# Kernel tuning notes

Hardware: AMD Instinct MI355X
Metric: run time of the kernel (lower is better)

The kernel has to match this reference:

```python
import jax, jax.numpy as jnp
import numpy as np
import math

DIM = 1024
NUM_HEADS = 16
SHARED_HEADS = 1
ROUTED_HEADS = 3
HEAD_DIM = DIM // NUM_HEADS
B, N = 2, 2048


def setup_inputs() -> dict:
    key = jax.random.key(0)
    ks = jax.random.split(key, 16)
    s = 1.0 / math.sqrt(DIM)
    inp = {
        "x": jax.random.normal(ks[0], (B, N, DIM), dtype=jnp.float32),
        "Wq": jax.random.uniform(ks[1], (DIM, DIM), minval=-s, maxval=s),
        "bq": jax.random.uniform(ks[2], (DIM,), minval=-s, maxval=s),
        "Wk": jax.random.uniform(ks[3], (DIM, DIM), minval=-s, maxval=s),
        "bk": jax.random.uniform(ks[4], (DIM,), minval=-s, maxval=s),
        "Wv": jax.random.uniform(ks[5], (DIM, DIM), minval=-s, maxval=s),
        "bv": jax.random.uniform(ks[6], (DIM,), minval=-s, maxval=s),
        "Wp": jax.random.uniform(ks[7], (DIM, DIM), minval=-s, maxval=s),
        "bp": jax.random.uniform(ks[8], (DIM,), minval=-s, maxval=s),
        "Wr": jax.random.uniform(ks[9], (NUM_HEADS - SHARED_HEADS, DIM), minval=-s, maxval=s),
        "br": jax.random.uniform(ks[10], (NUM_HEADS - SHARED_HEADS,), minval=-s, maxval=s),
        "Ws": jax.random.uniform(ks[11], (2, DIM), minval=-s, maxval=s),
        "bs": jax.random.uniform(ks[12], (2,), minval=-s, maxval=s),
        # temperature init: log(exp(1/0.24)-1), shape (H,1,1)
        "temperature": jnp.full((NUM_HEADS, 1, 1), float(np.log(np.expm1(1.0 / 0.24))), dtype=jnp.float32),
        "query_embedding": 0.02 * jax.random.normal(ks[13], (NUM_HEADS, 1, HEAD_DIM), dtype=jnp.float32),
    }
    return inp


def reference(x, Wq, bq, Wk, bk, Wv, bv, Wp, bp, Wr, br, Ws, bs, temperature, query_embedding):
    Bsz, Nn, C = x.shape
    H, hd = NUM_HEADS, HEAD_DIM

    def heads(W, b):
        y = x @ W.T + b  # [B,N,C]
        return y.reshape(Bsz, Nn, H, hd).transpose(0, 2, 1, 3)  # [B,H,N,hd]

    q = heads(Wq, bq)
    k = heads(Wk, bk)
    v = heads(Wv, bv)

    q_norm = q / jnp.linalg.norm(q, axis=-1, keepdims=True)
    q_scaled = (q_norm + query_embedding[None]) * jax.nn.softplus(temperature)[None]
    attn = jnp.einsum("bhqd,bhkd->bhqk", q_scaled, k) / math.sqrt(hd)
    attn = jax.nn.softmax(attn, axis=-1)
    h = jnp.einsum("bhqk,bhkd->bhqd", attn, v)
    h = h.transpose(0, 2, 1, 3).reshape(Bsz, Nn, C)  # [B,N,C]

    # routed-head gating
    gates = jax.nn.softmax(h @ Wr.T + br, axis=-1)  # [B,N,H-shared]
    _, idx = jax.lax.top_k(gates, ROUTED_HEADS)
    # NOTE: original uses num_classes=num_heads-shared_heads for one_hot
    mask = jax.nn.one_hot(idx, H - SHARED_HEADS, dtype=gates.dtype).sum(axis=-2)
    routed_gates = gates * mask * ROUTED_HEADS

    sw = jax.nn.softmax(h @ Ws.T + bs, axis=-1)  # [B,N,2]
    shared_gates = sw * SHARED_HEADS
    weight_0 = sw * 2.0
    shared_gates = weight_0[..., 0:1] * shared_gates
    routed_gates = weight_0[..., 1:2] * routed_gates
    masked_gates = jnp.concatenate([shared_gates, routed_gates], axis=-1)

    # einsum('bnc,bnd->bnd') == per-token scalar sum over c times h
    out = h * masked_gates.sum(axis=-1, keepdims=True)
    return out @ Wp.T + bp
```

## Files before the change

kernel.cpp:

```cpp
#include <hip/hip_runtime.h>
#include <hip/hip_bf16.h>

typedef short s16x8 __attribute__((ext_vector_type(8)));
typedef float f32x4 __attribute__((ext_vector_type(4)));
typedef float f32x16 __attribute__((ext_vector_type(16)));

__device__ __forceinline__ float b2f(unsigned short u) {
    union { unsigned int i; float f; } v;
    v.i = ((unsigned int)u) << 16;
    return v.f;
}
__device__ __forceinline__ unsigned int pkbf16(float a, float b) {
    union { __hip_bfloat162 h; unsigned int u; } v;
    v.h = __float22bfloat162_rn(make_float2(a, b));
    return v.u;
}
__device__ __forceinline__ float fast_exp2(float x) {
#if __has_builtin(__builtin_amdgcn_exp2f)
    return __builtin_amdgcn_exp2f(x);
#else
    return exp2f(x);
#endif
}

__device__ __forceinline__ void gl_lds16(const unsigned short* g, unsigned short* l) {
    __builtin_amdgcn_global_load_lds(
        (const __attribute__((address_space(1))) void*)g,
        (__attribute__((address_space(3))) void*)l, 16, 0, 0);
}

__device__ __forceinline__ void perm32swap(unsigned int &a, unsigned int &b) {
    asm("v_permlane32_swap_b32 %0, %1" : "+v"(a), "+v"(b));
}

__device__ __forceinline__ s16x8 mk8(unsigned int a, unsigned int b,
                                     unsigned int c, unsigned int d) {
    union { uint4 u; s16x8 h; } v;
    v.u = make_uint4(a, b, c, d);
    return v.h;
}

__device__ __forceinline__ void cvt8(const float* __restrict__ s,
                                     unsigned short* __restrict__ d, int i) {
    const float* p = s + (size_t)i * 8;
    float4 a = *(const float4*)p;
    float4 b = *(const float4*)(p + 4);
    unsigned int u0 = pkbf16(a.x, a.y), u1 = pkbf16(a.z, a.w);
    unsigned int u2 = pkbf16(b.x, b.y), u3 = pkbf16(b.z, b.w);
    uint4 o = {u0, u1, u2, u3};
    *(uint4*)&d[(size_t)i * 8] = o;
}

__global__ __launch_bounds__(256) void cvt_main(
    const float* __restrict__ x,  const float* __restrict__ Wq,
    const float* __restrict__ Wk, const float* __restrict__ Wv,
    const float* __restrict__ Wr, const float* __restrict__ Ws,
    const float* __restrict__ bq, const float* __restrict__ bk,
    const float* __restrict__ bv,
    unsigned short* __restrict__ xb, unsigned short* __restrict__ wqkv,
    unsigned short* __restrict__ wg, float* __restrict__ bqkv)
{
    int blk = blockIdx.x, t = threadIdx.x;
    if (blk < 2048)      cvt8(x,  xb,             blk * 256 + t);
    else if (blk < 2560) cvt8(Wq, wqkv,           (blk - 2048) * 256 + t);
    else if (blk < 3072) cvt8(Wk, wqkv + 1048576, (blk - 2560) * 256 + t);
    else if (blk < 3584) cvt8(Wv, wqkv + 2097152, (blk - 3072) * 256 + t);
    else if (blk < 3592) { int i = (blk - 3584) * 256 + t; if (i < 1920) cvt8(Wr, wg, i); }
    else if (blk < 3593) { int i = t; cvt8(Ws, wg + 15360, i); }
    else {
        int i = (blk - 3593) * 256 + t;
        bqkv[i] = (i < 1024) ? bq[i] : (i < 2048) ? bk[i - 1024] : bv[i - 2048];
    }
}

__global__ __launch_bounds__(256) void qkv_gemm(
    const unsigned short* __restrict__ A,
    const unsigned short* __restrict__ Bw,
    const float* __restrict__ bias,
    unsigned short* __restrict__ Q, unsigned short* __restrict__ K,
    unsigned short* __restrict__ Vt)
{
    __shared__ __attribute__((aligned(16))) unsigned short As[128 * 64];
    __shared__ __attribute__((aligned(16))) unsigned short Bs[128 * 64];
    const int t = threadIdx.x;
    const int wave = t >> 6, lane = t & 63;
    const int m0 = blockIdx.x * 128, n0 = blockIdx.y * 128;
    const int wm = (wave >> 1) * 64, wn = (wave & 1) * 64;
    const int lr = lane & 15, lq = lane >> 4;
    const int srow = lane >> 3;
    const int scol = (((lane & 7) ^ srow) << 3);

    f32x4 acc[4][4];
#pragma unroll
    for (int i = 0; i < 4; ++i)
#pragma unroll
        for (int j = 0; j < 4; ++j) acc[i][j] = (f32x4){0.f, 0.f, 0.f, 0.f};

    for (int k0 = 0; k0 < 1024; k0 += 64) {
        __syncthreads();
#pragma unroll
        for (int i = 0; i < 4; ++i) {
            int rb = wave * 32 + i * 8;
            gl_lds16(&A[(size_t)(m0 + rb + srow) * 1024 + k0 + scol], &As[rb * 64]);
            gl_lds16(&Bw[(size_t)(n0 + rb + srow) * 1024 + k0 + scol], &Bs[rb * 64]);
        }
        __syncthreads();
#pragma unroll
        for (int kk = 0; kk < 64; kk += 32) {
            const int po = ((((kk >> 3) + lq) ^ (lr & 7)) << 3);
            s16x8 af[4], bf[4];
#pragma unroll
            for (int i = 0; i < 4; ++i)
                af[i] = *(const s16x8*)&As[(wm + i * 16 + lr) * 64 + po];
#pragma unroll
            for (int j = 0; j < 4; ++j)
                bf[j] = *(const s16x8*)&Bs[(wn + j * 16 + lr) * 64 + po];
#pragma unroll
            for (int i = 0; i < 4; ++i)
#pragma unroll
                for (int j = 0; j < 4; ++j)
                    acc[i][j] = __builtin_amdgcn_mfma_f32_16x16x32_bf16(af[i], bf[j], acc[i][j], 0, 0, 0);
        }
    }
    const int kind = n0 >> 10;
    const int nc = n0 & 1023;
    if (kind < 2) {
        unsigned short* Cm = kind ? K : Q;
#pragma unroll
        for (int j = 0; j < 4; ++j) {
            int cl = wn + j * 16 + lr;
            float bv = bias[n0 + cl];
#pragma unroll
            for (int i = 0; i < 4; ++i) {
                int rowb = m0 + wm + i * 16 + lq * 4;
                unsigned int u0 = pkbf16(acc[i][j][0] + bv, acc[i][j][1] + bv);
                unsigned int u1 = pkbf16(acc[i][j][2] + bv, acc[i][j][3] + bv);
                Cm[(size_t)(rowb + 0) * 1024 + nc + cl] = (unsigned short)u0;
                Cm[(size_t)(rowb + 1) * 1024 + nc + cl] = (unsigned short)(u0 >> 16);
                Cm[(size_t)(rowb + 2) * 1024 + nc + cl] = (unsigned short)u1;
                Cm[(size_t)(rowb + 3) * 1024 + nc + cl] = (unsigned short)(u1 >> 16);
            }
        }
    } else {
        const int bb = m0 >> 11;
#pragma unroll
        for (int j = 0; j < 4; ++j) {
            int col = nc + wn + j * 16 + lr;
            int hh = col >> 6, dd = col & 63;
            float bv = bias[n0 + wn + j * 16 + lr];
#pragma unroll
            for (int i = 0; i < 4; ++i) {
                int tokb = m0 + wm + i * 16 + lq * 4;
                int tloc = tokb & 2047;
                uint2 u;
                u.x = pkbf16(acc[i][j][0] + bv, acc[i][j][1] + bv);
                u.y = pkbf16(acc[i][j][2] + bv, acc[i][j][3] + bv);
                *(uint2*)&Vt[((size_t)(bb * 16 + hh) * 64 + dd) * 2048 + tloc] = u;
            }
        }
    }
}

__global__ __launch_bounds__(512, 4) void attn_kernel(
    const unsigned short* __restrict__ Q,
    const unsigned short* __restrict__ Kb,
    const unsigned short* __restrict__ Vt,
    const float* __restrict__ temp,
    const float* __restrict__ qe,
    unsigned short* __restrict__ Hout)
{
    __shared__ __attribute__((aligned(16))) unsigned short Ks[2][2][64 * 64];
    __shared__ __attribute__((aligned(16))) unsigned short Vs[2][2][64 * 64];
    __shared__ float Lred[8][32];
    const int t = threadIdx.x, wave = t >> 6, lane = t & 63;
    const int ws = wave >> 2, wq = wave & 3;
    const int l31 = lane & 31, hi = lane >> 5;
    const int bh = blockIdx.x, b = bh >> 4, h = bh & 15;
    const int q0 = blockIdx.y * 128;
    const int srow = lane >> 3;
    const int scol = (((lane & 7) ^ srow) << 3);
    const int kbase = ws << 10;
    unsigned short* KsF = &Ks[0][0][0];

    auto stageK = [&](int kc, int cb) {
#pragma unroll
        for (int i2 = 0; i2 < 2; ++i2) {
            int rb = wq * 16 + i2 * 8;
            gl_lds16(&Kb[(size_t)(b * 2048 + kbase + kc + rb + srow) * 1024 + h * 64 + scol],
                     &Ks[ws][cb][rb * 64]);
        }
    };
    auto stageV = [&](int kc, int cb) {
#pragma unroll
        for (int i2 = 0; i2 < 2; ++i2) {
            int rb = wq * 16 + i2 * 8;
            gl_lds16(&Vt[((size_t)(b * 16 + h) * 64 + rb + srow) * 2048 + kbase + kc + scol],
                     &Vs[ws][cb][rb * 64]);
        }
    };

    {
        int rb = wave * 16;
        gl_lds16(&Q[(size_t)(b * 2048 + q0 + rb + srow) * 1024 + h * 64 + scol],
                 &KsF[rb * 64]);
        gl_lds16(&Q[(size_t)(b * 2048 + q0 + rb + 8 + srow) * 1024 + h * 64 + scol],
                 &KsF[(rb + 8) * 64]);
    }
    __syncthreads();

    s16x8 qf[4];
#pragma unroll
    for (int kd = 0; kd < 4; ++kd)
        qf[kd] = *(const s16x8*)&KsF[(wq * 32 + l31) * 64 + (((kd * 2 + hi) ^ (l31 & 7)) << 3)];
    __syncthreads();

    stageK(0, 0);
    stageV(0, 0);

    float tv = temp[h];
    float sp = ((tv > 20.f) ? tv : log1pf(__expf(tv))) * 0.18033688f;
    s16x8 aqB[4];
    {
        float v[4][8];
        float ss = 0.f;
#pragma unroll
        for (int kd = 0; kd < 4; ++kd)
#pragma unroll
            for (int e = 0; e < 8; ++e) {
                v[kd][e] = b2f((unsigned short)qf[kd][e]);
                ss += v[kd][e] * v[kd][e];
            }
        ss += __shfl_xor(ss, 32);
        float rn = rsqrtf(ss);
#pragma unroll
        for (int kd = 0; kd < 4; ++kd) {
            const float* qh = qe + h * 64 + kd * 16 + hi * 8;
            unsigned int w0 = pkbf16((v[kd][0] * rn + qh[0]) * sp, (v[kd][1] * rn + qh[1]) * sp);
            unsigned int w1 = pkbf16((v[kd][2] * rn + qh[2]) * sp, (v[kd][3] * rn + qh[3]) * sp);
            unsigned int w2 = pkbf16((v[kd][4] * rn + qh[4]) * sp, (v[kd][5] * rn + qh[5]) * sp);
            unsigned int w3 = pkbf16((v[kd][6] * rn + qh[6]) * sp, (v[kd][7] * rn + qh[7]) * sp);
            aqB[kd] = mk8(w0, w1, w2, w3);
        }
    }

    f32x16 accO[2];
#pragma unroll
    for (int r = 0; r < 16; ++r) { accO[0][r] = 0.f; accO[1][r] = 0.f; }
    float lsum = 0.f;

    for (int it = 0; it < 16; ++it) {
        const int c = it & 1;
        __syncthreads();
        if (it < 15) { stageK((it + 1) * 64, c ^ 1); stageV((it + 1) * 64, c ^ 1); }

#pragma unroll
        for (int jj = 0; jj < 2; ++jj) {
            const int j = jj ^ (wave & 1);

            s16x8 kf[4];
#pragma unroll
            for (int kd = 0; kd < 4; ++kd)
                kf[kd] = *(const s16x8*)&Ks[ws][c][(j * 32 + l31) * 64 + (((kd * 2 + hi) ^ (l31 & 7)) << 3)];
            f32x16 s;
#pragma unroll
            for (int r = 0; r < 16; ++r) s[r] = 0.f;
            __builtin_amdgcn_s_setprio(1);
#pragma unroll
            for (int kd = 0; kd < 4; ++kd)
                s = __builtin_amdgcn_mfma_f32_32x32x16_bf16(kf[kd], aqB[kd], s, 0, 0, 0);
            __builtin_amdgcn_s_setprio(0);

            float p[16];
#pragma unroll
            for (int r = 0; r < 16; ++r) p[r] = fast_exp2(s[r]);
            lsum += (((p[0] + p[1]) + (p[2] + p[3])) + ((p[4] + p[5]) + (p[6] + p[7])))
                  + (((p[8] + p[9]) + (p[10] + p[11])) + ((p[12] + p[13]) + (p[14] + p[15])));
            unsigned int u[8];
#pragma unroll
            for (int g = 0; g < 8; ++g) u[g] = pkbf16(p[2 * g], p[2 * g + 1]);

#pragma unroll
            for (int kh = 0; kh < 2; ++kh) {
                unsigned int a0 = u[4 * kh + 0], b0 = u[4 * kh + 2];
                unsigned int a1 = u[4 * kh + 1], b1 = u[4 * kh + 3];
                perm32swap(a0, b0);
                perm32swap(a1, b1);
                s16x8 pf = mk8(a0, a1, b0, b1);
                const int vb = (((j * 4 + kh * 2 + hi) ^ (l31 & 7)) << 3);
                s16x8 v0 = *(const s16x8*)&Vs[ws][c][(l31) * 64 + vb];
                s16x8 v1 = *(const s16x8*)&Vs[ws][c][(32 + l31) * 64 + vb];
                __builtin_amdgcn_s_setprio(1);
                accO[0] = __builtin_amdgcn_mfma_f32_32x32x16_bf16(pf, v0, accO[0], 0, 0, 0);
                accO[1] = __builtin_amdgcn_mfma_f32_32x32x16_bf16(pf, v1, accO[1], 0, 0, 0);
                __builtin_amdgcn_s_setprio(0);
            }
        }
    }

    lsum += __shfl_xor(lsum, 32);
    if (hi == 0) Lred[wave][l31] = lsum;
    __syncthreads();

    float* mb = (wq < 2) ? (float*)&Ks[0][wq][0] : (float*)&Vs[0][wq - 2][0];
    if (ws == 1) {
#pragma unroll
        for (int jd = 0; jd < 2; ++jd)
#pragma unroll
            for (int rg = 0; rg < 4; ++rg) {
                f32x4 vv = { accO[jd][rg * 4 + 0], accO[jd][rg * 4 + 1],
                             accO[jd][rg * 4 + 2], accO[jd][rg * 4 + 3] };
                *(f32x4*)&mb[((jd * 4 + rg) << 8) + (lane << 2)] = vv;
            }
    }
    __syncthreads();
    if (ws == 0) {
#pragma unroll
        for (int jd = 0; jd < 2; ++jd)
#pragma unroll
            for (int rg = 0; rg < 4; ++rg) {
                f32x4 vv = *(const f32x4*)&mb[((jd * 4 + rg) << 8) + (lane << 2)];
                accO[jd][rg * 4 + 0] += vv[0];
                accO[jd][rg * 4 + 1] += vv[1];
                accO[jd][rg * 4 + 2] += vv[2];
                accO[jd][rg * 4 + 3] += vv[3];
            }
#pragma unroll
        for (int jd = 0; jd < 2; ++jd)
#pragma unroll
            for (int r = 0; r < 16; ++r) {
                int qrow = (r & 3) + 8 * (r >> 2) + 4 * hi;
                float inv = 1.f / (Lred[wq][qrow] + Lred[wq + 4][qrow]);
                float val = accO[jd][r] * inv;
                Hout[(size_t)(b * 2048 + q0 + wq * 32 + qrow) * 1024 + h * 64 + jd * 32 + l31] =
                    (unsigned short)pkbf16(val, val);
            }
    }
}

__global__ __launch_bounds__(256) void gate_g(
    const unsigned short* __restrict__ Hb,
    const unsigned short* __restrict__ Wg,
    const float* __restrict__ br, const float* __restrict__ bs,
    const float* __restrict__ Wp, unsigned short* __restrict__ wpb,
    float* __restrict__ g)
{
    __shared__ __attribute__((aligned(16))) unsigned short As[4][16 * 64];
    __shared__ __attribute__((aligned(16))) unsigned short Gs[4][32 * 64];
    __shared__ float Lred[4][16][32];
    const int t = threadIdx.x, wave = t >> 6, lane = t & 63;
    const int lr = lane & 15, lq = lane >> 4;
    const int m0 = blockIdx.x * 16;
    const int srow = lane >> 3;
    const int scol = (((lane & 7) ^ srow) << 3);

    cvt8(Wp, wpb, blockIdx.x * 512 + t);
    cvt8(Wp, wpb, blockIdx.x * 512 + 256 + t);

    f32x4 acc[2];
    acc[0] = (f32x4){0.f, 0.f, 0.f, 0.f};
    acc[1] = (f32x4){0.f, 0.f, 0.f, 0.f};

    for (int k0 = wave * 64; k0 < 1024; k0 += 256) {
        gl_lds16(&Hb[(size_t)(m0 + srow) * 1024 + k0 + scol], &As[wave][0]);
        gl_lds16(&Hb[(size_t)(m0 + 8 + srow) * 1024 + k0 + scol], &As[wave][8 * 64]);
#pragma unroll
        for (int i = 0; i < 4; ++i) {
            int row = i * 8 + srow;
            int wr = (row > 16) ? 16 : row;
            gl_lds16(&Wg[(size_t)wr * 1024 + k0 + scol], &Gs[wave][i * 8 * 64]);
        }
        asm volatile("s_waitcnt vmcnt(0)" ::: "memory");
#pragma unroll
        for (int kk = 0; kk < 64; kk += 32) {
            const int po = ((((kk >> 3) + lq) ^ (lr & 7)) << 3);
            s16x8 af = *(const s16x8*)&As[wave][lr * 64 + po];
#pragma unroll
            for (int j = 0; j < 2; ++j) {
                s16x8 gf = *(const s16x8*)&Gs[wave][(j * 16 + lr) * 64 + po];
                acc[j] = __builtin_amdgcn_mfma_f32_16x16x32_bf16(af, gf, acc[j], 0, 0, 0);
            }
        }
    }
#pragma unroll
    for (int j = 0; j < 2; ++j)
#pragma unroll
        for (int r = 0; r < 4; ++r)
            Lred[wave][lq * 4 + r][j * 16 + lr] = acc[j][r];
    __syncthreads();
    if (t < 16) {
        float lg[17];
#pragma unroll
        for (int j = 0; j < 17; ++j)
            lg[j] = Lred[0][t][j] + Lred[1][t][j] + Lred[2][t][j] + Lred[3][t][j]
                  + ((j < 15) ? br[j] : bs[j - 15]);
        float mx = lg[0];
#pragma unroll
        for (int j = 1; j < 15; ++j) mx = fmaxf(mx, lg[j]);
        float sum = 0.f, v1 = -1.f, v2 = -1.f, v3 = -1.f;
#pragma unroll
        for (int j = 0; j < 15; ++j) {
            float e = __expf(lg[j] - mx);
            sum += e;
            if (e > v1)      { v3 = v2; v2 = v1; v1 = e; }
            else if (e > v2) { v3 = v2; v2 = e; }
            else if (e > v3) { v3 = e; }
        }
        float tops = (v1 + v2 + v3) / sum;
        float sm = fmaxf(lg[15], lg[16]);
        float e0 = __expf(lg[15] - sm), e1 = __expf(lg[16] - sm);
        float inv = 1.f / (e0 + e1);
        g[m0 + t] = 2.f * (e0 * inv) + 6.f * (e1 * inv) * tops;
    }
}

__global__ __launch_bounds__(256) void gemm64_out(
    const unsigned short* __restrict__ A,
    const unsigned short* __restrict__ Bw,
    const float* __restrict__ bias,
    const float* __restrict__ g,
    float* __restrict__ C)
{
    __shared__ __attribute__((aligned(16))) unsigned short As[2][64 * 64];
    __shared__ __attribute__((aligned(16))) unsigned short Bs[2][64 * 64];
    const int t = threadIdx.x, wave = t >> 6, lane = t & 63;
    const int lr = lane & 15, lq = lane >> 4;
    const int m0 = blockIdx.x * 64, n0 = blockIdx.y * 64;
    const int wm = (wave >> 1) * 32, wn = (wave & 1) * 32;
    const int srow = lane >> 3;
    const int scol = (((lane & 7) ^ srow) << 3);

    auto stage = [&](int k0, int cb) {
#pragma unroll
        for (int i = 0; i < 2; ++i) {
            int rb = wave * 16 + i * 8;
            gl_lds16(&A[(size_t)(m0 + rb + srow) * 1024 + k0 + scol], &As[cb][rb * 64]);
            gl_lds16(&Bw[(size_t)(n0 + rb + srow) * 1024 + k0 + scol], &Bs[cb][rb * 64]);
        }
    };

    f32x4 acc[2][2];
#pragma unroll
    for (int i = 0; i < 2; ++i)
#pragma unroll
        for (int j = 0; j < 2; ++j) acc[i][j] = (f32x4){0.f, 0.f, 0.f, 0.f};

    stage(0, 0);
    for (int it = 0; it < 16; ++it) {
        const int c = it & 1;
        __syncthreads();
        if (it < 15) stage((it + 1) * 64, c ^ 1);
#pragma unroll
        for (int kk = 0; kk < 64; kk += 32) {
            const int po = ((((kk >> 3) + lq) ^ (lr & 7)) << 3);
            s16x8 af[2], bf[2];
#pragma unroll
            for (int i = 0; i < 2; ++i)
                af[i] = *(const s16x8*)&As[c][(wm + i * 16 + lr) * 64 + po];
#pragma unroll
            for (int j = 0; j < 2; ++j)
                bf[j] = *(const s16x8*)&Bs[c][(wn + j * 16 + lr) * 64 + po];
#pragma unroll
            for (int i = 0; i < 2; ++i)
#pragma unroll
                for (int j = 0; j < 2; ++j)
                    acc[i][j] = __builtin_amdgcn_mfma_f32_16x16x32_bf16(af[i], bf[j], acc[i][j], 0, 0, 0);
        }
    }
#pragma unroll
    for (int i = 0; i < 2; ++i) {
        const float4 gi = *(const float4*)&g[m0 + wm + i * 16 + lq * 4];
        float gv[4] = {gi.x, gi.y, gi.z, gi.w};
#pragma unroll
        for (int j = 0; j < 2; ++j) {
            int col = n0 + wn + j * 16 + lr;
            float bv = bias[col];
            int rowb = m0 + wm + i * 16 + lq * 4;
#pragma unroll
            for (int r = 0; r < 4; ++r)
                C[(size_t)(rowb + r) * 1024 + col] = acc[i][j][r] * gv[r] + bv;
        }
    }
}

extern "C" void kernel_launch(void* const* d_in, const int* in_sizes, int n_in,
                              void* d_out, int out_size, void* d_ws, size_t ws_size,
                              hipStream_t stream)
{
    (void)in_sizes; (void)n_in; (void)out_size; (void)ws_size;
    const float* x   = (const float*)d_in[0];
    const float* Wq  = (const float*)d_in[1];
    const float* bq  = (const float*)d_in[2];
    const float* Wk  = (const float*)d_in[3];
    const float* bk  = (const float*)d_in[4];
    const float* Wv  = (const float*)d_in[5];
    const float* bv  = (const float*)d_in[6];
    const float* Wp  = (const float*)d_in[7];
    const float* bp  = (const float*)d_in[8];
    const float* Wr  = (const float*)d_in[9];
    const float* br  = (const float*)d_in[10];
    const float* Ws  = (const float*)d_in[11];
    const float* bs  = (const float*)d_in[12];
    const float* temperature = (const float*)d_in[13];
    const float* qe  = (const float*)d_in[14];
    float* out = (float*)d_out;

    const size_t MB = 1048576;
    unsigned short* qb   = (unsigned short*)d_ws;
    unsigned short* kb   = (unsigned short*)((char*)d_ws + 8 * MB);
    unsigned short* hb   = (unsigned short*)((char*)d_ws + 16 * MB);
    unsigned short* wqkv = (unsigned short*)((char*)d_ws + 24 * MB);
    unsigned short* wg   = (unsigned short*)((char*)d_ws + 30 * MB);
    float*          bqkv = (float*)((char*)d_ws + 30 * MB + 65536);
    float*          gbuf = (float*)((char*)d_ws + 30 * MB + 131072);
    unsigned short* xb = (unsigned short*)d_out;
    unsigned short* vt = xb + 4 * MB;
    unsigned short* wpb = qb;

    dim3 blk(256);
    cvt_main<<<dim3(3605), blk, 0, stream>>>(x, Wq, Wk, Wv, Wr, Ws, bq, bk, bv,
                                             xb, wqkv, wg, bqkv);
    qkv_gemm<<<dim3(32, 24), blk, 0, stream>>>(xb, wqkv, bqkv, qb, kb, vt);
    attn_kernel<<<dim3(32, 16), dim3(512), 0, stream>>>(qb, kb, vt, temperature, qe, hb);
    gate_g<<<dim3(256), blk, 0, stream>>>(hb, wg, br, bs, Wp, wpb, gbuf);
    gemm64_out<<<dim3(64, 16), blk, 0, stream>>>(hb, wpb, bp, gbuf, out);
}
```

Before: 213.0 us.

## Double-buffer QKV GEMM with BK=32 and remap block IDs for XCD locality

```diff
diff --git a/kernel.cpp b/kernel.cpp
--- a/kernel.cpp
+++ b/kernel.cpp
@@ -80,15 +80,26 @@
     unsigned short* __restrict__ Q, unsigned short* __restrict__ K,
     unsigned short* __restrict__ Vt)
 {
-    __shared__ __attribute__((aligned(16))) unsigned short As[128 * 64];
-    __shared__ __attribute__((aligned(16))) unsigned short Bs[128 * 64];
+    __shared__ __attribute__((aligned(16))) unsigned short As[2][128 * 32];
+    __shared__ __attribute__((aligned(16))) unsigned short Bs[2][128 * 32];
     const int t = threadIdx.x;
     const int wave = t >> 6, lane = t & 63;
-    const int m0 = blockIdx.x * 128, n0 = blockIdx.y * 128;
+    int bid = blockIdx.y * 32 + blockIdx.x;
+    bid = (bid & 7) * 96 + (bid >> 3);
+    const int m0 = (bid & 31) * 128, n0 = (bid >> 5) * 128;
     const int wm = (wave >> 1) * 64, wn = (wave & 1) * 64;
     const int lr = lane & 15, lq = lane >> 4;
-    const int srow = lane >> 3;
-    const int scol = (((lane & 7) ^ srow) << 3);
+    const int srow = lane >> 2;
+    const int scol = (((lane & 3) ^ (srow & 3)) << 3);
+
+    auto stage = [&](int k0, int cb) {
+#pragma unroll
+        for (int i = 0; i < 2; ++i) {
+            int rb = wave * 32 + i * 16;
+            gl_lds16(&A[(size_t)(m0 + rb + srow) * 1024 + k0 + scol], &As[cb][rb * 32]);
+            gl_lds16(&Bw[(size_t)(n0 + rb + srow) * 1024 + k0 + scol], &Bs[cb][rb * 32]);
+        }
+    };
 
     f32x4 acc[4][4];
 #pragma unroll
@@ -96,31 +107,24 @@
 #pragma unroll
         for (int j = 0; j < 4; ++j) acc[i][j] = (f32x4){0.f, 0.f, 0.f, 0.f};
 
-    for (int k0 = 0; k0 < 1024; k0 += 64) {
+    stage(0, 0);
+    for (int it = 0; it < 32; ++it) {
+        const int c = it & 1;
         __syncthreads();
-#pragma unroll
-        for (int i = 0; i < 4; ++i) {
-            int rb = wave * 32 + i * 8;
-            gl_lds16(&A[(size_t)(m0 + rb + srow) * 1024 + k0 + scol], &As[rb * 64]);
-            gl_lds16(&Bw[(size_t)(n0 + rb + srow) * 1024 + k0 + scol], &Bs[rb * 64]);
-        }
-        __syncthreads();
-#pragma unroll
-        for (int kk = 0; kk < 64; kk += 32) {
-            const int po = ((((kk >> 3) + lq) ^ (lr & 7)) << 3);
-            s16x8 af[4], bf[4];
-#pragma unroll
-            for (int i = 0; i < 4; ++i)
-                af[i] = *(const s16x8*)&As[(wm + i * 16 + lr) * 64 + po];
+        if (it < 31) stage((it + 1) * 32, c ^ 1);
+        const int po = ((lq ^ (lr & 3)) << 3);
+        s16x8 af[4], bf[4];
+#pragma unroll
+        for (int i = 0; i < 4; ++i)
+            af[i] = *(const s16x8*)&As[c][(wm + i * 16 + lr) * 32 + po];
+#pragma unroll
+        for (int j = 0; j < 4; ++j)
+            bf[j] = *(const s16x8*)&Bs[c][(wn + j * 16 + lr) * 32 + po];
+#pragma unroll
+        for (int i = 0; i < 4; ++i)
 #pragma unroll
             for (int j = 0; j < 4; ++j)
-                bf[j] = *(const s16x8*)&Bs[(wn + j * 16 + lr) * 64 + po];
-#pragma unroll
-            for (int i = 0; i < 4; ++i)
-#pragma unroll
-                for (int j = 0; j < 4; ++j)
-                    acc[i][j] = __builtin_amdgcn_mfma_f32_16x16x32_bf16(af[i], bf[j], acc[i][j], 0, 0, 0);
-        }
+                acc[i][j] = __builtin_amdgcn_mfma_f32_16x16x32_bf16(af[i], bf[j], acc[i][j], 0, 0, 0);
     }
     const int kind = n0 >> 10;
     const int nc = n0 & 1023;
@@ -424,7 +428,9 @@
     __shared__ __attribute__((aligned(16))) unsigned short Bs[2][64 * 64];
     const int t = threadIdx.x, wave = t >> 6, lane = t & 63;
     const int lr = lane & 15, lq = lane >> 4;
-    const int m0 = blockIdx.x * 64, n0 = blockIdx.y * 64;
+    int bid = blockIdx.y * 64 + blockIdx.x;
+    bid = (bid & 7) * 128 + (bid >> 3);
+    const int m0 = (bid & 63) * 64, n0 = (bid >> 6) * 64;
     const int wm = (wave >> 1) * 32, wn = (wave & 1) * 32;
     const int srow = lane >> 3;
     const int scol = (((lane & 7) ^ srow) << 3);
```

Result: no change. 215.6 us (+1.2%).

## Fuse gate computation and Wp bf16 conversion into output projection GEMM

Applied to the files above, without the earlier changes.

```diff
diff --git a/kernel.cpp b/kernel.cpp
--- a/kernel.cpp
+++ b/kernel.cpp
@@ -337,62 +337,118 @@
     }
 }
 
-__global__ __launch_bounds__(256) void gate_g(
-    const unsigned short* __restrict__ Hb,
+__global__ __launch_bounds__(256, 4) void gemm64_out(
+    const unsigned short* __restrict__ A,
+    const float* __restrict__ Wp,
+    const float* __restrict__ bias,
     const unsigned short* __restrict__ Wg,
     const float* __restrict__ br, const float* __restrict__ bs,
-    const float* __restrict__ Wp, unsigned short* __restrict__ wpb,
-    float* __restrict__ g)
+    float* __restrict__ C)
 {
-    __shared__ __attribute__((aligned(16))) unsigned short As[4][16 * 64];
-    __shared__ __attribute__((aligned(16))) unsigned short Gs[4][32 * 64];
-    __shared__ float Lred[4][16][32];
+    __shared__ __attribute__((aligned(16))) unsigned short As[2][64 * 64];
+    __shared__ __attribute__((aligned(16))) unsigned short Bs[2][64 * 64];
+    __shared__ float Gred[64][18];
+    __shared__ float gv[64];
     const int t = threadIdx.x, wave = t >> 6, lane = t & 63;
     const int lr = lane & 15, lq = lane >> 4;
-    const int m0 = blockIdx.x * 16;
+    const int m0 = blockIdx.x * 64, n0 = blockIdx.y * 64;
+    const int wm = (wave >> 1) * 32, wn = (wave & 1) * 32;
+    const int cg = wave & 1;
     const int srow = lane >> 3;
     const int scol = (((lane & 7) ^ srow) << 3);
-
-    cvt8(Wp, wpb, blockIdx.x * 512 + t);
-    cvt8(Wp, wpb, blockIdx.x * 512 + 256 + t);
-
-    f32x4 acc[2];
-    acc[0] = (f32x4){0.f, 0.f, 0.f, 0.f};
-    acc[1] = (f32x4){0.f, 0.f, 0.f, 0.f};
-
-    for (int k0 = wave * 64; k0 < 1024; k0 += 256) {
-        gl_lds16(&Hb[(size_t)(m0 + srow) * 1024 + k0 + scol], &As[wave][0]);
-        gl_lds16(&Hb[(size_t)(m0 + 8 + srow) * 1024 + k0 + scol], &As[wave][8 * 64]);
-#pragma unroll
-        for (int i = 0; i < 4; ++i) {
-            int row = i * 8 + srow;
-            int wr = (row > 16) ? 16 : row;
-            gl_lds16(&Wg[(size_t)wr * 1024 + k0 + scol], &Gs[wave][i * 8 * 64]);
-        }
-        asm volatile("s_waitcnt vmcnt(0)" ::: "memory");
+    const int brow = lane >> 2;
+    const int bc0 = (lane & 3) * 16;
+
+    auto stageA = [&](int k0, int cb) {
+#pragma unroll
+        for (int i = 0; i < 2; ++i) {
+            int rb = wave * 16 + i * 8;
+            gl_lds16(&A[(size_t)(m0 + rb + srow) * 1024 + k0 + scol], &As[cb][rb * 64]);
+        }
+    };
+
+    float4 bl[4];
+    auto loadB = [&](int k0) {
+        const float* p = &Wp[(size_t)(n0 + wave * 16 + brow) * 1024 + k0 + bc0];
+        bl[0] = ((const float4*)p)[0];
+        bl[1] = ((const float4*)p)[1];
+        bl[2] = ((const float4*)p)[2];
+        bl[3] = ((const float4*)p)[3];
+    };
+    auto writeB = [&](int cb) {
+        int row = wave * 16 + brow;
+        int lb = (lane & 3) * 2;
+        uint4 w0 = { pkbf16(bl[0].x, bl[0].y), pkbf16(bl[0].z, bl[0].w),
+                     pkbf16(bl[1].x, bl[1].y), pkbf16(bl[1].z, bl[1].w) };
+        uint4 w1 = { pkbf16(bl[2].x, bl[2].y), pkbf16(bl[2].z, bl[2].w),
+                     pkbf16(bl[3].x, bl[3].y), pkbf16(bl[3].z, bl[3].w) };
+        *(uint4*)&Bs[cb][row * 64 + (((lb    ) ^ (row & 7)) << 3)] = w0;
+        *(uint4*)&Bs[cb][row * 64 + (((lb + 1) ^ (row & 7)) << 3)] = w1;
+    };
+    auto loadWg = [&](int k0, s16x8* wf) {
+        wf[0] = *(const s16x8*)&Wg[(size_t)(cg * 16 + lr) * 1024 + k0 + 0  + lq * 8];
+        wf[1] = *(const s16x8*)&Wg[(size_t)(cg * 16 + lr) * 1024 + k0 + 32 + lq * 8];
+    };
+
+    f32x4 acc[2][2];
+#pragma unroll
+    for (int i = 0; i < 2; ++i)
+#pragma unroll
+        for (int j = 0; j < 2; ++j) acc[i][j] = (f32x4){0.f, 0.f, 0.f, 0.f};
+    f32x4 gacc[2];
+    gacc[0] = (f32x4){0.f, 0.f, 0.f, 0.f};
+    gacc[1] = (f32x4){0.f, 0.f, 0.f, 0.f};
+
+    s16x8 wgc[2], wgn[2];
+    stageA(0, 0);
+    loadB(0); writeB(0);
+    loadWg(0, wgc);
+
+    for (int it = 0; it < 16; ++it) {
+        const int c = it & 1;
+        __syncthreads();
+        if (it < 15) {
+            stageA((it + 1) * 64, c ^ 1);
+            loadB((it + 1) * 64);
+            loadWg((it + 1) * 64, wgn);
+        }
 #pragma unroll
         for (int kk = 0; kk < 64; kk += 32) {
             const int po = ((((kk >> 3) + lq) ^ (lr & 7)) << 3);
-            s16x8 af = *(const s16x8*)&As[wave][lr * 64 + po];
-#pragma unroll
-            for (int j = 0; j < 2; ++j) {
-                s16x8 gf = *(const s16x8*)&Gs[wave][(j * 16 + lr) * 64 + po];
-                acc[j] = __builtin_amdgcn_mfma_f32_16x16x32_bf16(af, gf, acc[j], 0, 0, 0);
-            }
-        }
-    }
-#pragma unroll
-    for (int j = 0; j < 2; ++j)
-#pragma unroll
-        for (int r = 0; r < 4; ++r)
-            Lred[wave][lq * 4 + r][j * 16 + lr] = acc[j][r];
+            s16x8 af[2], bf[2];
+#pragma unroll
+            for (int i = 0; i < 2; ++i)
+                af[i] = *(const s16x8*)&As[c][(wm + i * 16 + lr) * 64 + po];
+#pragma unroll
+            for (int j = 0; j < 2; ++j)
+                bf[j] = *(const s16x8*)&Bs[c][(wn + j * 16 + lr) * 64 + po];
+#pragma unroll
+            for (int i = 0; i < 2; ++i)
+#pragma unroll
+                for (int j = 0; j < 2; ++j)
+                    acc[i][j] = __builtin_amdgcn_mfma_f32_16x16x32_bf16(af[i], bf[j], acc[i][j], 0, 0, 0);
+            gacc[0] = __builtin_amdgcn_mfma_f32_16x16x32_bf16(af[0], wgc[kk >> 5], gacc[0], 0, 0, 0);
+            gacc[1] = __builtin_amdgcn_mfma_f32_16x16x32_bf16(af[1], wgc[kk >> 5], gacc[1], 0, 0, 0);
+        }
+        if (it < 15) {
+            writeB(c ^ 1);
+            wgc[0] = wgn[0]; wgc[1] = wgn[1];
+        }
+    }
+
+#pragma unroll
+    for (int i = 0; i < 2; ++i)
+#pragma unroll
+        for (int r = 0; r < 4; ++r) {
+            int col = cg * 16 + lr;
+            if (col < 17) Gred[wm + i * 16 + lq * 4 + r][col] = gacc[i][r];
+        }
     __syncthreads();
-    if (t < 16) {
+    if (t < 64) {
         float lg[17];
 #pragma unroll
         for (int j = 0; j < 17; ++j)
-            lg[j] = Lred[0][t][j] + Lred[1][t][j] + Lred[2][t][j] + Lred[3][t][j]
-                  + ((j < 15) ? br[j] : bs[j - 15]);
+            lg[j] = Gred[t][j] + ((j < 15) ? br[j] : bs[j - 15]);
         float mx = lg[0];
 #pragma unroll
         for (int j = 1; j < 15; ++j) mx = fmaxf(mx, lg[j]);
@@ -409,75 +465,22 @@
         float sm = fmaxf(lg[15], lg[16]);
         float e0 = __expf(lg[15] - sm), e1 = __expf(lg[16] - sm);
         float inv = 1.f / (e0 + e1);
-        g[m0 + t] = 2.f * (e0 * inv) + 6.f * (e1 * inv) * tops;
-    }
-}
-
-__global__ __launch_bounds__(256) void gemm64_out(
-    const unsigned short* __restrict__ A,
-    const unsigned short* __restrict__ Bw,
-    const float* __restrict__ bias,
-    const float* __restrict__ g,
-    float* __restrict__ C)
-{
-    __shared__ __attribute__((aligned(16))) unsigned short As[2][64 * 64];
-    __shared__ __attribute__((aligned(16))) unsigned short Bs[2][64 * 64];
-    const int t = threadIdx.x, wave = t >> 6, lane = t & 63;
-    const int lr = lane & 15, lq = lane >> 4;
-    const int m0 = blockIdx.x * 64, n0 = blockIdx.y * 64;
-    const int wm = (wave >> 1) * 32, wn = (wave & 1) * 32;
-    const int srow = lane >> 3;
-    const int scol = (((lane & 7) ^ srow) << 3);
-
-    auto stage = [&](int k0, int cb) {
-#pragma unroll
-        for (int i = 0; i < 2; ++i) {
-            int rb = wave * 16 + i * 8;
-            gl_lds16(&A[(size_t)(m0 + rb + srow) * 1024 + k0 + scol], &As[cb][rb * 64]);
-            gl_lds16(&Bw[(size_t)(n0 + rb + srow) * 1024 + k0 + scol], &Bs[cb][rb * 64]);
-        }
-    };
-
-    f32x4 acc[2][2];
-#pragma unroll
-    for (int i = 0; i < 2; ++i)
-#pragma unroll
-        for (int j = 0; j < 2; ++j) acc[i][j] = (f32x4){0.f, 0.f, 0.f, 0.f};
-
-    stage(0, 0);
-    for (int it = 0; it < 16; ++it) {
-        const int c = it & 1;
-        __syncthreads();
-        if (it < 15) stage((it + 1) * 64, c ^ 1);
-#pragma unroll
-        for (int kk = 0; kk < 64; kk += 32) {
-            const int po = ((((kk >> 3) + lq) ^ (lr & 7)) << 3);
-            s16x8 af[2], bf[2];
-#pragma unroll
-            for (int i = 0; i < 2; ++i)
-                af[i] = *(const s16x8*)&As[c][(wm + i * 16 + lr) * 64 + po];
-#pragma unroll
-            for (int j = 0; j < 2; ++j)
-                bf[j] = *(const s16x8*)&Bs[c][(wn + j * 16 + lr) * 64 + po];
-#pragma unroll
-            for (int i = 0; i < 2; ++i)
-#pragma unroll
-                for (int j = 0; j < 2; ++j)
-                    acc[i][j] = __builtin_amdgcn_mfma_f32_16x16x32_bf16(af[i], bf[j], acc[i][j], 0, 0, 0);
-        }
-    }
+        gv[t] = 2.f * (e0 * inv) + 6.f * (e1 * inv) * tops;
+    }
+    __syncthreads();
+
 #pragma unroll
     for (int i = 0; i < 2; ++i) {
-        const float4 gi = *(const float4*)&g[m0 + wm + i * 16 + lq * 4];
-        float gv[4] = {gi.x, gi.y, gi.z, gi.w};
+        int rowl = wm + i * 16 + lq * 4;
+        float g0 = gv[rowl], g1 = gv[rowl + 1], g2 = gv[rowl + 2], g3 = gv[rowl + 3];
+        float gvr[4] = {g0, g1, g2, g3};
 #pragma unroll
         for (int j = 0; j < 2; ++j) {
             int col = n0 + wn + j * 16 + lr;
             float bv = bias[col];
-            int rowb = m0 + wm + i * 16 + lq * 4;
 #pragma unroll
             for (int r = 0; r < 4; ++r)
-                C[(size_t)(rowb + r) * 1024 + col] = acc[i][j][r] * gv[r] + bv;
+                C[(size_t)(m0 + rowl + r) * 1024 + col] = acc[i][j][r] * gvr[r] + bv;
         }
     }
 }
@@ -511,16 +514,13 @@
     unsigned short* wqkv = (unsigned short*)((char*)d_ws + 24 * MB);
     unsigned short* wg   = (unsigned short*)((char*)d_ws + 30 * MB);
     float*          bqkv = (float*)((char*)d_ws + 30 * MB + 65536);
-    float*          gbuf = (float*)((char*)d_ws + 30 * MB + 131072);
     unsigned short* xb = (unsigned short*)d_out;
     unsigned short* vt = xb + 4 * MB;
-    unsigned short* wpb = qb;
 
     dim3 blk(256);
     cvt_main<<<dim3(3605), blk, 0, stream>>>(x, Wq, Wk, Wv, Wr, Ws, bq, bk, bv,
                                              xb, wqkv, wg, bqkv);
     qkv_gemm<<<dim3(32, 24), blk, 0, stream>>>(xb, wqkv, bqkv, qb, kb, vt);
     attn_kernel<<<dim3(32, 16), dim3(512), 0, stream>>>(qb, kb, vt, temperature, qe, hb);
-    gate_g<<<dim3(256), blk, 0, stream>>>(hb, wg, br, bs, Wp, wpb, gbuf);
-    gemm64_out<<<dim3(64, 16), blk, 0, stream>>>(hb, wpb, bp, gbuf, out);
-}
+    gemm64_out<<<dim3(64, 16), blk, 0, stream>>>(hb, Wp, bp, wg, br, bs, out);
+}
```

Measured after the change: 234.2 us. 1.1x slower.
